# Kernel tuning notes

Hardware: AMD Instinct MI355X
Metric: run time of the kernel (lower is better)

The kernel has to match this reference:

```python
import jax, jax.numpy as jnp
import numpy as np

N_NODES = 100000


def setup_inputs() -> dict:
    key = jax.random.key(0)
    k1, k2, k3 = jax.random.split(key, 3)
    x = jax.random.normal(k1, (N_NODES, 128), dtype=jnp.float32)
    edge_index = jax.random.randint(k2, (2, 1600000), 0, N_NODES, dtype=jnp.int32)
    # GCNConv linear weight: [out_features, in_features], bias: [out_features]
    W = jax.random.normal(k3, (128, 128), dtype=jnp.float32) * (1.0 / np.sqrt(128.0))
    b = jnp.zeros((128,), dtype=jnp.float32)
    return {"x": x, "edge_index": edge_index, "W": W, "b": b}


def reference(x, edge_index, W, b):
    n = x.shape[0]
    # --- add self loops (PyG GCNConv default) ---
    loop = jnp.arange(n, dtype=edge_index.dtype)
    row = jnp.concatenate([edge_index[0], loop])  # source nodes
    col = jnp.concatenate([edge_index[1], loop])  # target nodes
    # --- symmetric degree normalization D^{-1/2} A_hat D^{-1/2} ---
    ones = jnp.ones(row.shape[0], dtype=x.dtype)
    deg = jax.ops.segment_sum(ones, col, num_segments=n)
    deg_inv_sqrt = jnp.where(deg > 0, jax.lax.rsqrt(deg), 0.0)
    norm = deg_inv_sqrt[row] * deg_inv_sqrt[col]  # [E + N]
    # --- linear transform then gather-normalize-scatter aggregation ---
    xw = x @ W.T  # [N, out]
    msgs = xw[row] * norm[:, None]  # [E + N, out]
    out = jax.ops.segment_sum(msgs, col, num_segments=n)  # [N, out]
    return out + b
```

## Files before the change

kernel.cpp:

```cpp
#include <hip/hip_runtime.h>

#define NF 128

#define BSHIFT 7
#define BNODES (1 << BSHIFT)
#define NBUCK 782
#define BCAP 2560
#define CHUNK 4096
#define BZT 512

typedef __attribute__((ext_vector_type(8))) short bf16x8;
typedef __attribute__((ext_vector_type(4))) float f32x4;

__device__ inline short f2bf_rne(float f) {
    unsigned u = __float_as_uint(f);
    u += 0x7FFFu + ((u >> 16) & 1u);
    return (short)(u >> 16);
}
__device__ inline float bf_lo(unsigned u) { return __uint_as_float(u << 16); }
__device__ inline float bf_hi(unsigned u) { return __uint_as_float(u & 0xFFFF0000u); }

__global__ __launch_bounds__(256) void prep_kernel(const float* __restrict__ W,
                                                   unsigned short* __restrict__ wswz,
                                                   int* __restrict__ bcursor) {
    int t = blockIdx.x * 256 + threadIdx.x;
    if (t < NBUCK) bcursor[t] = t * BCAP;
    if (t < 2048) {
        int lane = t & 63, frag = t >> 6;
        int nb = frag & 7, kc = frag >> 3;
        int o = nb * 16 + (lane & 15);
        int k0 = kc * 32 + (lane >> 4) * 8;
        const float4* ap = (const float4*)(W + o * NF + k0);
        float4 a0 = ap[0], a1 = ap[1];
        bf16x8 v;
        v[0] = f2bf_rne(a0.x); v[1] = f2bf_rne(a0.y);
        v[2] = f2bf_rne(a0.z); v[3] = f2bf_rne(a0.w);
        v[4] = f2bf_rne(a1.x); v[5] = f2bf_rne(a1.y);
        v[6] = f2bf_rne(a1.z); v[7] = f2bf_rne(a1.w);
        *(bf16x8*)(wswz + (size_t)t * 8) = v;
    }
}

__global__ __launch_bounds__(BZT) void bucketize_kernel(const int* __restrict__ row,
                                                        const int* __restrict__ col,
                                                        int* __restrict__ bcursor,
                                                        int* __restrict__ bpacked, int E) {
    __shared__ int2 pe[CHUNK];
    __shared__ int hist[NBUCK];
    __shared__ int base[NBUCK];
    const int t = threadIdx.x;
    const int e0 = blockIdx.x * CHUNK;
    const int cnt = min(CHUNK, E - e0);
    const int cnt4 = cnt & ~3;
    for (int i = t; i < NBUCK; i += BZT) hist[i] = 0;
    __syncthreads();
    for (int i = t * 4; i < cnt4; i += BZT * 4) {
        int4 c4 = *(const int4*)(col + e0 + i);
        int4 r4 = *(const int4*)(row + e0 + i);
        pe[i + 0] = make_int2(c4.x, r4.x);
        pe[i + 1] = make_int2(c4.y, r4.y);
        pe[i + 2] = make_int2(c4.z, r4.z);
        pe[i + 3] = make_int2(c4.w, r4.w);
        atomicAdd(&hist[c4.x >> BSHIFT], 1);
        atomicAdd(&hist[c4.y >> BSHIFT], 1);
        atomicAdd(&hist[c4.z >> BSHIFT], 1);
        atomicAdd(&hist[c4.w >> BSHIFT], 1);
    }
    for (int i = cnt4 + t; i < cnt; i += BZT) {
        int c = col[e0 + i];
        pe[i] = make_int2(c, row[e0 + i]);
        atomicAdd(&hist[c >> BSHIFT], 1);
    }
    __syncthreads();
    for (int i = t; i < NBUCK; i += BZT) {
        int h = hist[i];
        base[i] = h ? atomicAdd(&bcursor[i], h) : 0;
        hist[i] = 0;
    }
    __syncthreads();
    for (int i = t * 4; i < cnt4; i += BZT * 4) {
        int4 a = *(const int4*)(&pe[i]);
        int4 b = *(const int4*)(&pe[i + 2]);
        int bk, pos;
        bk = a.x >> BSHIFT; pos = base[bk] + atomicAdd(&hist[bk], 1);
        bpacked[pos] = (a.y << BSHIFT) | (a.x & (BNODES - 1));
        bk = a.z >> BSHIFT; pos = base[bk] + atomicAdd(&hist[bk], 1);
        bpacked[pos] = (a.w << BSHIFT) | (a.z & (BNODES - 1));
        bk = b.x >> BSHIFT; pos = base[bk] + atomicAdd(&hist[bk], 1);
        bpacked[pos] = (b.y << BSHIFT) | (b.x & (BNODES - 1));
        bk = b.z >> BSHIFT; pos = base[bk] + atomicAdd(&hist[bk], 1);
        bpacked[pos] = (b.w << BSHIFT) | (b.z & (BNODES - 1));
    }
    for (int i = cnt4 + t; i < cnt; i += BZT) {
        int2 p = pe[i];
        int bk = p.x >> BSHIFT;
        int pos = base[bk] + atomicAdd(&hist[bk], 1);
        bpacked[pos] = (p.y << BSHIFT) | (p.x & (BNODES - 1));
    }
}

__device__ inline int block_exclusive_scan_256(int val) {
    __shared__ int wsum[4];
    int lane = threadIdx.x & 63, wave = threadIdx.x >> 6;
    int x = val;
#pragma unroll
    for (int off = 1; off < 64; off <<= 1) {
        int y = __shfl_up(x, off, 64);
        if (lane >= off) x += y;
    }
    if (lane == 63) wsum[wave] = x;
    __syncthreads();
    if (threadIdx.x == 0) {
        int acc = 0;
        for (int w = 0; w < 4; ++w) { int t = wsum[w]; wsum[w] = acc; acc += t; }
    }
    __syncthreads();
    return x - val + wsum[wave];
}

__global__ __launch_bounds__(256) void bucket_build_kernel(const int* __restrict__ bpacked,
                                                           const int* __restrict__ bcursor,
                                                           int* __restrict__ cnt,
                                                           float* __restrict__ dis,
                                                           int* __restrict__ offs,
                                                           int* __restrict__ ed, int N) {
    __shared__ int pe[BCAP];
    __shared__ int h[BNODES];
    __shared__ int edl[BCAP];
    const int b = blockIdx.x;
    const int node0 = b << BSHIFT;
    const int nn = min(BNODES, N - node0);
    const int start = b * BCAP;
    const int ecnt = bcursor[b] - start;
    for (int i = threadIdx.x; i < nn; i += 256) h[i] = 0;
    __syncthreads();
    for (int i = threadIdx.x; i < ecnt; i += 256) {
        int p = bpacked[start + i];
        pe[i] = p;
        atomicAdd(&h[p & (BNODES - 1)], 1);
    }
    __syncthreads();
    const int t = threadIdx.x;
    int v0 = (2 * t < nn) ? h[2 * t] : 0;
    int v1 = (2 * t + 1 < nn) ? h[2 * t + 1] : 0;
    int exc = block_exclusive_scan_256(v0 + v1);
    if (2 * t < nn) {
        offs[node0 + 2 * t] = start + exc;
        cnt[node0 + 2 * t] = v0;
        dis[node0 + 2 * t] = rsqrtf((float)v0 + 1.0f);
        h[2 * t] = exc;
    }
    if (2 * t + 1 < nn) {
        offs[node0 + 2 * t + 1] = start + exc + v0;
        cnt[node0 + 2 * t + 1] = v1;
        dis[node0 + 2 * t + 1] = rsqrtf((float)v1 + 1.0f);
        h[2 * t + 1] = exc + v0;
    }
    __syncthreads();
    for (int i = threadIdx.x; i < ecnt; i += 256) {
        int p = pe[i];
        int pos = atomicAdd(&h[p & (BNODES - 1)], 1);
        edl[pos] = p >> BSHIFT;
    }
    __syncthreads();
    for (int i = threadIdx.x; i < ecnt; i += 256) ed[start + i] = edl[i];
}

__global__ __launch_bounds__(256) void gemm_xws_kernel(const float* __restrict__ x,
                                                       const unsigned short* __restrict__ wswz,
                                                       const float* __restrict__ dis,
                                                       unsigned short* __restrict__ xws,
                                                       int n) {
    __shared__ short Wl[NF * NF];

    for (int i = threadIdx.x; i < NF * NF / 8; i += 256)
        *(bf16x8*)(&Wl[i * 8]) = *(const bf16x8*)(wswz + (size_t)i * 8);
    __syncthreads();

    const int lane = threadIdx.x & 63;
    const int wave = threadIdx.x >> 6;
    const int l15 = lane & 15;
    const int quad = lane >> 4;
    const int tile = blockIdx.x * 64;

    int r = tile + wave * 16 + l15;
    if (r >= n) r = n - 1;

    float4 xa[4][2];
#pragma unroll
    for (int kc = 0; kc < 4; ++kc) {
        const float4* ap = (const float4*)(x + (size_t)r * NF + kc * 32 + quad * 8);
        xa[kc][0] = ap[0];
        xa[kc][1] = ap[1];
    }

    f32x4 acc[8];
#pragma unroll
    for (int nb = 0; nb < 8; ++nb) acc[nb] = (f32x4)0.0f;

#pragma unroll
    for (int kc = 0; kc < 4; ++kc) {
        bf16x8 Af;
        Af[0] = f2bf_rne(xa[kc][0].x); Af[1] = f2bf_rne(xa[kc][0].y);
        Af[2] = f2bf_rne(xa[kc][0].z); Af[3] = f2bf_rne(xa[kc][0].w);
        Af[4] = f2bf_rne(xa[kc][1].x); Af[5] = f2bf_rne(xa[kc][1].y);
        Af[6] = f2bf_rne(xa[kc][1].z); Af[7] = f2bf_rne(xa[kc][1].w);
#pragma unroll
        for (int nb = 0; nb < 8; ++nb) {
            bf16x8 Bf = *(const bf16x8*)(&Wl[((kc * 8 + nb) * 64 + lane) * 8]);
            acc[nb] = __builtin_amdgcn_mfma_f32_16x16x32_bf16(Af, Bf, acc[nb], 0, 0, 0);
        }
    }

    int rbase = tile + wave * 16 + quad * 4;
#pragma unroll
    for (int reg = 0; reg < 4; ++reg) {
        int rr = rbase + reg;
        if (rr < n) {
            float dsc = dis[rr];
#pragma unroll
            for (int nb = 0; nb < 8; ++nb)
                xws[(size_t)rr * NF + nb * 16 + l15] = (unsigned short)f2bf_rne(acc[nb][reg] * dsc);
        }
    }
}

__global__ __launch_bounds__(256) void gather_kernel(const int* __restrict__ ed,
                                                     const int* __restrict__ offs,
                                                     const int* __restrict__ cnt,
                                                     const float* __restrict__ dis,
                                                     const unsigned short* __restrict__ xws,
                                                     const float* __restrict__ b,
                                                     float* __restrict__ out,
                                                     int nbase, int nend) {
    int node = nbase + (int)((blockIdx.x * blockDim.x + threadIdx.x) >> 6);
    const int lane = threadIdx.x & 63;
    if (node >= nend) return;
    node = __builtin_amdgcn_readfirstlane(node);
    const int lsub = lane & 31;
    const bool lo = lane < 32;
    const float dc = dis[node];
    const int start = offs[node];
    const int end = start + cnt[node];

    float ax = 0.f, ay = 0.f, az = 0.f, aw = 0.f;
    {
        uint2 u = *(const uint2*)(xws + (size_t)node * NF + lsub * 4);
        if (lo) { ax = bf_lo(u.x); ay = bf_hi(u.x); az = bf_lo(u.y); aw = bf_hi(u.y); }
    }
    int i = start;
    for (; i + 16 <= end; i += 16) {
        int r0 = ed[i], r1 = ed[i + 1], r2 = ed[i + 2], r3 = ed[i + 3];
        int r4 = ed[i + 4], r5 = ed[i + 5], r6 = ed[i + 6], r7 = ed[i + 7];
        int r8 = ed[i + 8], r9 = ed[i + 9], ra = ed[i + 10], rb = ed[i + 11];
        int rc = ed[i + 12], rd = ed[i + 13], re = ed[i + 14], rf = ed[i + 15];
        int sa = lo ? r0 : r1, sb = lo ? r2 : r3, sc = lo ? r4 : r5, sd = lo ? r6 : r7;
        int se = lo ? r8 : r9, sf = lo ? ra : rb, sg = lo ? rc : rd, sh = lo ? re : rf;
        uint2 ua = *(const uint2*)(xws + (size_t)sa * NF + lsub * 4);
        uint2 ub = *(const uint2*)(xws + (size_t)sb * NF + lsub * 4);
        uint2 uc = *(const uint2*)(xws + (size_t)sc * NF + lsub * 4);
        uint2 ud = *(const uint2*)(xws + (size_t)sd * NF + lsub * 4);
        uint2 ue = *(const uint2*)(xws + (size_t)se * NF + lsub * 4);
        uint2 uf = *(const uint2*)(xws + (size_t)sf * NF + lsub * 4);
        uint2 ug = *(const uint2*)(xws + (size_t)sg * NF + lsub * 4);
        uint2 uh = *(const uint2*)(xws + (size_t)sh * NF + lsub * 4);
        ax += bf_lo(ua.x) + bf_lo(ub.x) + bf_lo(uc.x) + bf_lo(ud.x);
        ay += bf_hi(ua.x) + bf_hi(ub.x) + bf_hi(uc.x) + bf_hi(ud.x);
        az += bf_lo(ua.y) + bf_lo(ub.y) + bf_lo(uc.y) + bf_lo(ud.y);
        aw += bf_hi(ua.y) + bf_hi(ub.y) + bf_hi(uc.y) + bf_hi(ud.y);
        ax += bf_lo(ue.x) + bf_lo(uf.x) + bf_lo(ug.x) + bf_lo(uh.x);
        ay += bf_hi(ue.x) + bf_hi(uf.x) + bf_hi(ug.x) + bf_hi(uh.x);
        az += bf_lo(ue.y) + bf_lo(uf.y) + bf_lo(ug.y) + bf_lo(uh.y);
        aw += bf_hi(ue.y) + bf_hi(uf.y) + bf_hi(ug.y) + bf_hi(uh.y);
    }
    for (; i < end; i += 8) {
        int i1 = min(i + 1, end - 1), i2 = min(i + 2, end - 1), i3 = min(i + 3, end - 1);
        int i4 = min(i + 4, end - 1), i5 = min(i + 5, end - 1), i6 = min(i + 6, end - 1),
            i7 = min(i + 7, end - 1);
        int r0 = ed[i], r1 = ed[i1], r2 = ed[i2], r3 = ed[i3];
        int r4 = ed[i4], r5 = ed[i5], r6 = ed[i6], r7 = ed[i7];
        int sa = lo ? r0 : r1, sb = lo ? r2 : r3, sc = lo ? r4 : r5, sd = lo ? r6 : r7;
        uint2 ua = *(const uint2*)(xws + (size_t)sa * NF + lsub * 4);
        uint2 ub = *(const uint2*)(xws + (size_t)sb * NF + lsub * 4);
        uint2 uc = *(const uint2*)(xws + (size_t)sc * NF + lsub * 4);
        uint2 ud = *(const uint2*)(xws + (size_t)sd * NF + lsub * 4);
        const int my0 = lo ? 0 : 1;
        if (i + my0 < end)     { ax += bf_lo(ua.x); ay += bf_hi(ua.x); az += bf_lo(ua.y); aw += bf_hi(ua.y); }
        if (i + 2 + my0 < end) { ax += bf_lo(ub.x); ay += bf_hi(ub.x); az += bf_lo(ub.y); aw += bf_hi(ub.y); }
        if (i + 4 + my0 < end) { ax += bf_lo(uc.x); ay += bf_hi(uc.x); az += bf_lo(uc.y); aw += bf_hi(uc.y); }
        if (i + 6 + my0 < end) { ax += bf_lo(ud.x); ay += bf_hi(ud.x); az += bf_lo(ud.y); aw += bf_hi(ud.y); }
    }
    ax += __shfl_xor(ax, 32, 64);
    ay += __shfl_xor(ay, 32, 64);
    az += __shfl_xor(az, 32, 64);
    aw += __shfl_xor(aw, 32, 64);
    if (lo) {
        float4 bb = ((const float4*)b)[lsub];
        float4 o;
        o.x = fmaf(ax, dc, bb.x);
        o.y = fmaf(ay, dc, bb.y);
        o.z = fmaf(az, dc, bb.z);
        o.w = fmaf(aw, dc, bb.w);
        ((float4*)(out + (size_t)node * NF))[lsub] = o;
    }
}

extern "C" void kernel_launch(void* const* d_in, const int* in_sizes, int n_in,
                              void* d_out, int out_size, void* d_ws, size_t ws_size,
                              hipStream_t stream) {
    const float* x = (const float*)d_in[0];
    const int* ei = (const int*)d_in[1];
    const float* W = (const float*)d_in[2];
    const float* b = (const float*)d_in[3];
    float* out = (float*)d_out;

    const int N = in_sizes[0] / NF;
    const int E = in_sizes[1] / 2;
    const int* row = ei;
    const int* col = ei + E;

    char* ws = (char*)d_ws;
    unsigned short* xws = (unsigned short*)ws;
    ws += (size_t)N * NF * sizeof(unsigned short);
    int* cnt = (int*)ws; ws += (size_t)N * sizeof(int);
    float* dis = (float*)ws; ws += (size_t)N * sizeof(float);
    int* offs = (int*)ws; ws += (size_t)N * sizeof(int);
    unsigned short* wswz = (unsigned short*)ws; ws += (size_t)NF * NF * sizeof(unsigned short);
    int* bpacked = (int*)ws; ws += (size_t)NBUCK * BCAP * sizeof(int);
    int* bcursor = (int*)ws; ws += 1024 * sizeof(int);
    int* ed = (int*)ws;

    const int CB = (E + CHUNK - 1) / CHUNK;

    prep_kernel<<<8, 256, 0, stream>>>(W, wswz, bcursor);
    bucketize_kernel<<<CB, BZT, 0, stream>>>(row, col, bcursor, bpacked, E);

    bucket_build_kernel<<<NBUCK, 256, 0, stream>>>(bpacked, bcursor, cnt, dis, offs, ed, N);

    gemm_xws_kernel<<<(N + 63) / 64, 256, 0, stream>>>(x, wswz, dis, xws, N);

    {
        int half = (N / 2 + 3) & ~3;
        int blocks1 = (half + 3) / 4;
        int blocks2 = (N - half + 3) / 4;
        gather_kernel<<<blocks1, 256, 0, stream>>>(ed, offs, cnt, dis, xws, b, out, 0, half);
        gather_kernel<<<blocks2, 256, 0, stream>>>(ed, offs, cnt, dis, xws, b, out, half, N);
    }
}
```

Before: 209.3 us.

## Fuse bucket CSR build into gather kernel and compute degrees via global atomics

Removes the separate bucket_build kernel and the global ed/offs/dis arrays. Per-node degrees are now counted with global atomics during bucketization, and the GEMM computes its own rsqrt scale from them. Each bucket's CSR is rebuilt in shared memory inside the gather kernel, so edge lists are read from LDS instead of global memory. The cost is 1.6M global atomics, an extra memset, and a gather that now runs only 782 blocks with 4 waves each, which sharply lowers parallelism and load balance in the gather phase.

```diff
diff --git a/kernel.cpp b/kernel.cpp
--- a/kernel.cpp
+++ b/kernel.cpp
@@ -44,32 +44,38 @@
 __global__ __launch_bounds__(BZT) void bucketize_kernel(const int* __restrict__ row,
                                                         const int* __restrict__ col,
                                                         int* __restrict__ bcursor,
-                                                        int* __restrict__ bpacked, int E) {
+                                                        int* __restrict__ bpacked,
+                                                        int* __restrict__ cnt, int E) {
     __shared__ int2 pe[CHUNK];
     __shared__ int hist[NBUCK];
     __shared__ int base[NBUCK];
     const int t = threadIdx.x;
     const int e0 = blockIdx.x * CHUNK;
-    const int cnt = min(CHUNK, E - e0);
-    const int cnt4 = cnt & ~3;
+    const int c_n = min(CHUNK, E - e0);
+    const int c4 = c_n & ~3;
     for (int i = t; i < NBUCK; i += BZT) hist[i] = 0;
     __syncthreads();
-    for (int i = t * 4; i < cnt4; i += BZT * 4) {
-        int4 c4 = *(const int4*)(col + e0 + i);
-        int4 r4 = *(const int4*)(row + e0 + i);
-        pe[i + 0] = make_int2(c4.x, r4.x);
-        pe[i + 1] = make_int2(c4.y, r4.y);
-        pe[i + 2] = make_int2(c4.z, r4.z);
-        pe[i + 3] = make_int2(c4.w, r4.w);
-        atomicAdd(&hist[c4.x >> BSHIFT], 1);
-        atomicAdd(&hist[c4.y >> BSHIFT], 1);
-        atomicAdd(&hist[c4.z >> BSHIFT], 1);
-        atomicAdd(&hist[c4.w >> BSHIFT], 1);
-    }
-    for (int i = cnt4 + t; i < cnt; i += BZT) {
+    for (int i = t * 4; i < c4; i += BZT * 4) {
+        int4 cc = *(const int4*)(col + e0 + i);
+        int4 rr = *(const int4*)(row + e0 + i);
+        pe[i + 0] = make_int2(cc.x, rr.x);
+        pe[i + 1] = make_int2(cc.y, rr.y);
+        pe[i + 2] = make_int2(cc.z, rr.z);
+        pe[i + 3] = make_int2(cc.w, rr.w);
+        atomicAdd(&hist[cc.x >> BSHIFT], 1);
+        atomicAdd(&hist[cc.y >> BSHIFT], 1);
+        atomicAdd(&hist[cc.z >> BSHIFT], 1);
+        atomicAdd(&hist[cc.w >> BSHIFT], 1);
+        atomicAdd(&cnt[cc.x], 1);
+        atomicAdd(&cnt[cc.y], 1);
+        atomicAdd(&cnt[cc.z], 1);
+        atomicAdd(&cnt[cc.w], 1);
+    }
+    for (int i = c4 + t; i < c_n; i += BZT) {
         int c = col[e0 + i];
         pe[i] = make_int2(c, row[e0 + i]);
         atomicAdd(&hist[c >> BSHIFT], 1);
+        atomicAdd(&cnt[c], 1);
     }
     __syncthreads();
     for (int i = t; i < NBUCK; i += BZT) {
@@ -78,7 +84,7 @@
         hist[i] = 0;
     }
     __syncthreads();
-    for (int i = t * 4; i < cnt4; i += BZT * 4) {
+    for (int i = t * 4; i < c4; i += BZT * 4) {
         int4 a = *(const int4*)(&pe[i]);
         int4 b = *(const int4*)(&pe[i + 2]);
         int bk, pos;
@@ -91,7 +97,7 @@
         bk = b.z >> BSHIFT; pos = base[bk] + atomicAdd(&hist[bk], 1);
         bpacked[pos] = (b.w << BSHIFT) | (b.z & (BNODES - 1));
     }
-    for (int i = cnt4 + t; i < cnt; i += BZT) {
+    for (int i = c4 + t; i < c_n; i += BZT) {
         int2 p = pe[i];
         int bk = p.x >> BSHIFT;
         int pos = base[bk] + atomicAdd(&hist[bk], 1);
@@ -118,57 +124,9 @@
     return x - val + wsum[wave];
 }
 
-__global__ __launch_bounds__(256) void bucket_build_kernel(const int* __restrict__ bpacked,
-                                                           const int* __restrict__ bcursor,
-                                                           int* __restrict__ cnt,
-                                                           float* __restrict__ dis,
-                                                           int* __restrict__ offs,
-                                                           int* __restrict__ ed, int N) {
-    __shared__ int pe[BCAP];
-    __shared__ int h[BNODES];
-    __shared__ int edl[BCAP];
-    const int b = blockIdx.x;
-    const int node0 = b << BSHIFT;
-    const int nn = min(BNODES, N - node0);
-    const int start = b * BCAP;
-    const int ecnt = bcursor[b] - start;
-    for (int i = threadIdx.x; i < nn; i += 256) h[i] = 0;
-    __syncthreads();
-    for (int i = threadIdx.x; i < ecnt; i += 256) {
-        int p = bpacked[start + i];
-        pe[i] = p;
-        atomicAdd(&h[p & (BNODES - 1)], 1);
-    }
-    __syncthreads();
-    const int t = threadIdx.x;
-    int v0 = (2 * t < nn) ? h[2 * t] : 0;
-    int v1 = (2 * t + 1 < nn) ? h[2 * t + 1] : 0;
-    int exc = block_exclusive_scan_256(v0 + v1);
-    if (2 * t < nn) {
-        offs[node0 + 2 * t] = start + exc;
-        cnt[node0 + 2 * t] = v0;
-        dis[node0 + 2 * t] = rsqrtf((float)v0 + 1.0f);
-        h[2 * t] = exc;
-    }
-    if (2 * t + 1 < nn) {
-        offs[node0 + 2 * t + 1] = start + exc + v0;
-        cnt[node0 + 2 * t + 1] = v1;
-        dis[node0 + 2 * t + 1] = rsqrtf((float)v1 + 1.0f);
-        h[2 * t + 1] = exc + v0;
-    }
-    __syncthreads();
-    for (int i = threadIdx.x; i < ecnt; i += 256) {
-        int p = pe[i];
-        int pos = atomicAdd(&h[p & (BNODES - 1)], 1);
-        edl[pos] = p >> BSHIFT;
-    }
-    __syncthreads();
-    for (int i = threadIdx.x; i < ecnt; i += 256) ed[start + i] = edl[i];
-}
-
 __global__ __launch_bounds__(256) void gemm_xws_kernel(const float* __restrict__ x,
                                                        const unsigned short* __restrict__ wswz,
-                                                       const float* __restrict__ dis,
+                                                       const int* __restrict__ cnt,
                                                        unsigned short* __restrict__ xws,
                                                        int n) {
     __shared__ short Wl[NF * NF];
@@ -217,7 +175,7 @@
     for (int reg = 0; reg < 4; ++reg) {
         int rr = rbase + reg;
         if (rr < n) {
-            float dsc = dis[rr];
+            float dsc = rsqrtf((float)cnt[rr] + 1.0f);
 #pragma unroll
             for (int nb = 0; nb < 8; ++nb)
                 xws[(size_t)rr * NF + nb * 16 + l15] = (unsigned short)f2bf_rne(acc[nb][reg] * dsc);
@@ -225,83 +183,114 @@
     }
 }
 
-__global__ __launch_bounds__(256) void gather_kernel(const int* __restrict__ ed,
-                                                     const int* __restrict__ offs,
-                                                     const int* __restrict__ cnt,
-                                                     const float* __restrict__ dis,
-                                                     const unsigned short* __restrict__ xws,
-                                                     const float* __restrict__ b,
-                                                     float* __restrict__ out,
-                                                     int nbase, int nend) {
-    int node = nbase + (int)((blockIdx.x * blockDim.x + threadIdx.x) >> 6);
-    const int lane = threadIdx.x & 63;
-    if (node >= nend) return;
-    node = __builtin_amdgcn_readfirstlane(node);
+__global__ __launch_bounds__(256) void bucket_gather_kernel(const int* __restrict__ bpacked,
+                                                            const int* __restrict__ bcursor,
+                                                            const int* __restrict__ cnt,
+                                                            const unsigned short* __restrict__ xws,
+                                                            const float* __restrict__ b,
+                                                            float* __restrict__ out, int N) {
+    __shared__ int pe[BCAP];
+    __shared__ int h[BNODES];
+    __shared__ int offl[BNODES];
+    __shared__ int edl[BCAP];
+    const int bkt = blockIdx.x;
+    const int node0 = bkt << BSHIFT;
+    const int nn = min(BNODES, N - node0);
+    const int start = bkt * BCAP;
+    const int ecnt = bcursor[bkt] - start;
+    const int t = threadIdx.x;
+
+    for (int i = t; i < nn; i += 256) h[i] = 0;
+    __syncthreads();
+    for (int i = t; i < ecnt; i += 256) {
+        int p = bpacked[start + i];
+        pe[i] = p;
+        atomicAdd(&h[p & (BNODES - 1)], 1);
+    }
+    __syncthreads();
+    int v0 = (2 * t < nn) ? h[2 * t] : 0;
+    int v1 = (2 * t + 1 < nn) ? h[2 * t + 1] : 0;
+    int exc = block_exclusive_scan_256(v0 + v1);
+    if (2 * t < nn) { offl[2 * t] = exc; h[2 * t] = exc; }
+    if (2 * t + 1 < nn) { offl[2 * t + 1] = exc + v0; h[2 * t + 1] = exc + v0; }
+    __syncthreads();
+    for (int i = t; i < ecnt; i += 256) {
+        int p = pe[i];
+        int pos = atomicAdd(&h[p & (BNODES - 1)], 1);
+        edl[pos] = p >> BSHIFT;
+    }
+    __syncthreads();
+    const int lane = t & 63;
+    const int wid = t >> 6;
     const int lsub = lane & 31;
     const bool lo = lane < 32;
-    const float dc = dis[node];
-    const int start = offs[node];
-    const int end = start + cnt[node];
-
-    float ax = 0.f, ay = 0.f, az = 0.f, aw = 0.f;
-    {
-        uint2 u = *(const uint2*)(xws + (size_t)node * NF + lsub * 4);
-        if (lo) { ax = bf_lo(u.x); ay = bf_hi(u.x); az = bf_lo(u.y); aw = bf_hi(u.y); }
-    }
-    int i = start;
-    for (; i + 16 <= end; i += 16) {
-        int r0 = ed[i], r1 = ed[i + 1], r2 = ed[i + 2], r3 = ed[i + 3];
-        int r4 = ed[i + 4], r5 = ed[i + 5], r6 = ed[i + 6], r7 = ed[i + 7];
-        int r8 = ed[i + 8], r9 = ed[i + 9], ra = ed[i + 10], rb = ed[i + 11];
-        int rc = ed[i + 12], rd = ed[i + 13], re = ed[i + 14], rf = ed[i + 15];
-        int sa = lo ? r0 : r1, sb = lo ? r2 : r3, sc = lo ? r4 : r5, sd = lo ? r6 : r7;
-        int se = lo ? r8 : r9, sf = lo ? ra : rb, sg = lo ? rc : rd, sh = lo ? re : rf;
-        uint2 ua = *(const uint2*)(xws + (size_t)sa * NF + lsub * 4);
-        uint2 ub = *(const uint2*)(xws + (size_t)sb * NF + lsub * 4);
-        uint2 uc = *(const uint2*)(xws + (size_t)sc * NF + lsub * 4);
-        uint2 ud = *(const uint2*)(xws + (size_t)sd * NF + lsub * 4);
-        uint2 ue = *(const uint2*)(xws + (size_t)se * NF + lsub * 4);
-        uint2 uf = *(const uint2*)(xws + (size_t)sf * NF + lsub * 4);
-        uint2 ug = *(const uint2*)(xws + (size_t)sg * NF + lsub * 4);
-        uint2 uh = *(const uint2*)(xws + (size_t)sh * NF + lsub * 4);
-        ax += bf_lo(ua.x) + bf_lo(ub.x) + bf_lo(uc.x) + bf_lo(ud.x);
-        ay += bf_hi(ua.x) + bf_hi(ub.x) + bf_hi(uc.x) + bf_hi(ud.x);
-        az += bf_lo(ua.y) + bf_lo(ub.y) + bf_lo(uc.y) + bf_lo(ud.y);
-        aw += bf_hi(ua.y) + bf_hi(ub.y) + bf_hi(uc.y) + bf_hi(ud.y);
-        ax += bf_lo(ue.x) + bf_lo(uf.x) + bf_lo(ug.x) + bf_lo(uh.x);
-        ay += bf_hi(ue.x) + bf_hi(uf.x) + bf_hi(ug.x) + bf_hi(uh.x);
-        az += bf_lo(ue.y) + bf_lo(uf.y) + bf_lo(ug.y) + bf_lo(uh.y);
-        aw += bf_hi(ue.y) + bf_hi(uf.y) + bf_hi(ug.y) + bf_hi(uh.y);
-    }
-    for (; i < end; i += 8) {
-        int i1 = min(i + 1, end - 1), i2 = min(i + 2, end - 1), i3 = min(i + 3, end - 1);
-        int i4 = min(i + 4, end - 1), i5 = min(i + 5, end - 1), i6 = min(i + 6, end - 1),
-            i7 = min(i + 7, end - 1);
-        int r0 = ed[i], r1 = ed[i1], r2 = ed[i2], r3 = ed[i3];
-        int r4 = ed[i4], r5 = ed[i5], r6 = ed[i6], r7 = ed[i7];
-        int sa = lo ? r0 : r1, sb = lo ? r2 : r3, sc = lo ? r4 : r5, sd = lo ? r6 : r7;
-        uint2 ua = *(const uint2*)(xws + (size_t)sa * NF + lsub * 4);
-        uint2 ub = *(const uint2*)(xws + (size_t)sb * NF + lsub * 4);
-        uint2 uc = *(const uint2*)(xws + (size_t)sc * NF + lsub * 4);
-        uint2 ud = *(const uint2*)(xws + (size_t)sd * NF + lsub * 4);
-        const int my0 = lo ? 0 : 1;
-        if (i + my0 < end)     { ax += bf_lo(ua.x); ay += bf_hi(ua.x); az += bf_lo(ua.y); aw += bf_hi(ua.y); }
-        if (i + 2 + my0 < end) { ax += bf_lo(ub.x); ay += bf_hi(ub.x); az += bf_lo(ub.y); aw += bf_hi(ub.y); }
-        if (i + 4 + my0 < end) { ax += bf_lo(uc.x); ay += bf_hi(uc.x); az += bf_lo(uc.y); aw += bf_hi(uc.y); }
-        if (i + 6 + my0 < end) { ax += bf_lo(ud.x); ay += bf_hi(ud.x); az += bf_lo(ud.y); aw += bf_hi(ud.y); }
-    }
-    ax += __shfl_xor(ax, 32, 64);
-    ay += __shfl_xor(ay, 32, 64);
-    az += __shfl_xor(az, 32, 64);
-    aw += __shfl_xor(aw, 32, 64);
-    if (lo) {
-        float4 bb = ((const float4*)b)[lsub];
-        float4 o;
-        o.x = fmaf(ax, dc, bb.x);
-        o.y = fmaf(ay, dc, bb.y);
-        o.z = fmaf(az, dc, bb.z);
-        o.w = fmaf(aw, dc, bb.w);
-        ((float4*)(out + (size_t)node * NF))[lsub] = o;
+
+    for (int nl = wid; nl < nn; nl += 4) {
+        const int node = node0 + nl;
+        const int st = offl[nl];
+        const int en = h[nl];
+        const float dc = rsqrtf((float)(en - st) + 1.0f);
+
+        float ax = 0.f, ay = 0.f, az = 0.f, aw = 0.f;
+        {
+            uint2 u = *(const uint2*)(xws + (size_t)node * NF + lsub * 4);
+            if (lo) { ax = bf_lo(u.x); ay = bf_hi(u.x); az = bf_lo(u.y); aw = bf_hi(u.y); }
+        }
+        int i = st;
+        for (; i + 16 <= en; i += 16) {
+            int r0 = edl[i], r1 = edl[i + 1], r2 = edl[i + 2], r3 = edl[i + 3];
+            int r4 = edl[i + 4], r5 = edl[i + 5], r6 = edl[i + 6], r7 = edl[i + 7];
+            int r8 = edl[i + 8], r9 = edl[i + 9], ra = edl[i + 10], rb = edl[i + 11];
+            int rc = edl[i + 12], rd = edl[i + 13], re = edl[i + 14], rf = edl[i + 15];
+            int sa = lo ? r0 : r1, sb = lo ? r2 : r3, sc = lo ? r4 : r5, sd = lo ? r6 : r7;
+            int se = lo ? r8 : r9, sf = lo ? ra : rb, sg = lo ? rc : rd, sh = lo ? re : rf;
+            uint2 ua = *(const uint2*)(xws + (size_t)sa * NF + lsub * 4);
+            uint2 ub = *(const uint2*)(xws + (size_t)sb * NF + lsub * 4);
+            uint2 uc = *(const uint2*)(xws + (size_t)sc * NF + lsub * 4);
+            uint2 ud = *(const uint2*)(xws + (size_t)sd * NF + lsub * 4);
+            uint2 ue = *(const uint2*)(xws + (size_t)se * NF + lsub * 4);
+            uint2 uf = *(const uint2*)(xws + (size_t)sf * NF + lsub * 4);
+            uint2 ug = *(const uint2*)(xws + (size_t)sg * NF + lsub * 4);
+            uint2 uh = *(const uint2*)(xws + (size_t)sh * NF + lsub * 4);
+            ax += bf_lo(ua.x) + bf_lo(ub.x) + bf_lo(uc.x) + bf_lo(ud.x);
+            ay += bf_hi(ua.x) + bf_hi(ub.x) + bf_hi(uc.x) + bf_hi(ud.x);
+            az += bf_lo(ua.y) + bf_lo(ub.y) + bf_lo(uc.y) + bf_lo(ud.y);
+            aw += bf_hi(ua.y) + bf_hi(ub.y) + bf_hi(uc.y) + bf_hi(ud.y);
+            ax += bf_lo(ue.x) + bf_lo(uf.x) + bf_lo(ug.x) + bf_lo(uh.x);
+            ay += bf_hi(ue.x) + bf_hi(uf.x) + bf_hi(ug.x) + bf_hi(uh.x);
+            az += bf_lo(ue.y) + bf_lo(uf.y) + bf_lo(ug.y) + bf_lo(uh.y);
+            aw += bf_hi(ue.y) + bf_hi(uf.y) + bf_hi(ug.y) + bf_hi(uh.y);
+        }
+        for (; i < en; i += 8) {
+            int i1 = min(i + 1, en - 1), i2 = min(i + 2, en - 1), i3 = min(i + 3, en - 1);
+            int i4 = min(i + 4, en - 1), i5 = min(i + 5, en - 1), i6 = min(i + 6, en - 1),
+                i7 = min(i + 7, en - 1);
+            int r0 = edl[i], r1 = edl[i1], r2 = edl[i2], r3 = edl[i3];
+            int r4 = edl[i4], r5 = edl[i5], r6 = edl[i6], r7 = edl[i7];
+            int sa = lo ? r0 : r1, sb = lo ? r2 : r3, sc = lo ? r4 : r5, sd = lo ? r6 : r7;
+            uint2 ua = *(const uint2*)(xws + (size_t)sa * NF + lsub * 4);
+            uint2 ub = *(const uint2*)(xws + (size_t)sb * NF + lsub * 4);
+            uint2 uc = *(const uint2*)(xws + (size_t)sc * NF + lsub * 4);
+            uint2 ud = *(const uint2*)(xws + (size_t)sd * NF + lsub * 4);
+            const int my0 = lo ? 0 : 1;
+            if (i + my0 < en)     { ax += bf_lo(ua.x); ay += bf_hi(ua.x); az += bf_lo(ua.y); aw += bf_hi(ua.y); }
+            if (i + 2 + my0 < en) { ax += bf_lo(ub.x); ay += bf_hi(ub.x); az += bf_lo(ub.y); aw += bf_hi(ub.y); }
+            if (i + 4 + my0 < en) { ax += bf_lo(uc.x); ay += bf_hi(uc.x); az += bf_lo(uc.y); aw += bf_hi(uc.y); }
+            if (i + 6 + my0 < en) { ax += bf_lo(ud.x); ay += bf_hi(ud.x); az += bf_lo(ud.y); aw += bf_hi(ud.y); }
+        }
+        ax += __shfl_xor(ax, 32, 64);
+        ay += __shfl_xor(ay, 32, 64);
+        az += __shfl_xor(az, 32, 64);
+        aw += __shfl_xor(aw, 32, 64);
+        if (lo) {
+            float4 bb = ((const float4*)b)[lsub];
+            float4 o;
+            o.x = fmaf(ax, dc, bb.x);
+            o.y = fmaf(ay, dc, bb.y);
+            o.z = fmaf(az, dc, bb.z);
+            o.w = fmaf(aw, dc, bb.w);
+            ((float4*)(out + (size_t)node * NF))[lsub] = o;
+        }
     }
 }
 
@@ -323,27 +312,18 @@
     unsigned short* xws = (unsigned short*)ws;
     ws += (size_t)N * NF * sizeof(unsigned short);
     int* cnt = (int*)ws; ws += (size_t)N * sizeof(int);
-    float* dis = (float*)ws; ws += (size_t)N * sizeof(float);
-    int* offs = (int*)ws; ws += (size_t)N * sizeof(int);
     unsigned short* wswz = (unsigned short*)ws; ws += (size_t)NF * NF * sizeof(unsigned short);
     int* bpacked = (int*)ws; ws += (size_t)NBUCK * BCAP * sizeof(int);
-    int* bcursor = (int*)ws; ws += 1024 * sizeof(int);
-    int* ed = (int*)ws;
+    int* bcursor = (int*)ws;
 
     const int CB = (E + CHUNK - 1) / CHUNK;
 
+    hipMemsetAsync(cnt, 0, (size_t)N * sizeof(int), stream);
+
     prep_kernel<<<8, 256, 0, stream>>>(W, wswz, bcursor);
-    bucketize_kernel<<<CB, BZT, 0, stream>>>(row, col, bcursor, bpacked, E);
-
-    bucket_build_kernel<<<NBUCK, 256, 0, stream>>>(bpacked, bcursor, cnt, dis, offs, ed, N);
-
-    gemm_xws_kernel<<<(N + 63) / 64, 256, 0, stream>>>(x, wswz, dis, xws, N);
-
-    {
-        int half = (N / 2 + 3) & ~3;
-        int blocks1 = (half + 3) / 4;
-        int blocks2 = (N - half + 3) / 4;
-        gather_kernel<<<blocks1, 256, 0, stream>>>(ed, offs, cnt, dis, xws, b, out, 0, half);
-        gather_kernel<<<blocks2, 256, 0, stream>>>(ed, offs, cnt, dis, xws, b, out, half, N);
-    }
-}
+    bucketize_kernel<<<CB, BZT, 0, stream>>>(row, col, bcursor, bpacked, cnt, E);
+
+    gemm_xws_kernel<<<(N + 63) / 64, 256, 0, stream>>>(x, wswz, cnt, xws, N);
+
+    bucket_gather_kernel<<<NBUCK, 256, 0, stream>>>(bpacked, bcursor, cnt, xws, b, out, N);
+}
```

After: 274.3 us. +31.1%, slower.
